# Kernel optimization log

Hardware: AMD Instinct MI355X
Metric: run time of the kernel (lower is better)

Reference implementation:

```python
import jax, jax.numpy as jnp
import numpy as np

N, IN_DIM, H, K = 4096, 64, 64, 3
DT = 0.05


def graph_filter(z, S_powers, W):
    # z: [N, d_in], S_powers: [K, N, N], W: [K, d_in, d_out]
    zk = jnp.einsum('knm,md->knd', S_powers, z)   # K-hop diffused features
    return jnp.einsum('knd,kde->ne', zk, W)       # sum over taps k


def setup_inputs() -> dict:
    key = jax.random.key(0)
    ks = jax.random.split(key, 8)
    w_scale = 0.1
    return {
        'x': jax.random.normal(ks[0], (N, H), jnp.float32),
        'u': jax.random.normal(ks[1], (N, IN_DIM), jnp.float32),
        'S_powers': jax.random.normal(ks[2], (K, N, N), jnp.float32) / np.float32(np.sqrt(N)),
        'WA_hat': jax.random.normal(ks[3], (K, H, H), jnp.float32) * w_scale,
        'WB_hat': jax.random.normal(ks[4], (K, IN_DIM, H), jnp.float32) * w_scale,
        'WA_state': jax.random.normal(ks[5], (K, H, H), jnp.float32) * w_scale,
        'WB_state': jax.random.normal(ks[6], (K, IN_DIM, H), jnp.float32) * w_scale,
        'bx': jnp.zeros((1, H), jnp.float32),
        'bu': jnp.zeros((1, H), jnp.float32),
        'b': jnp.ones((1, H), jnp.float32) * 0.1,
        'n_steps': 4,
    }


def reference(x, u, S_powers, WA_hat, WB_hat, WA_state, WB_state, bx, bu, b, n_steps):
    # Input-driven terms are constant across solver steps; hoist them.
    fu = jax.nn.relu(graph_filter(u, S_powers, WB_hat) + bu)   # [N, H]
    sigma_c = jnp.tanh(graph_filter(u, S_powers, WB_state))    # [N, H]

    def step(xc, _):
        f = jax.nn.relu(graph_filter(xc, S_powers, WA_hat) + bx) + fu
        dx = -(b + f) * xc - graph_filter(xc, S_powers, WA_state) + f * sigma_c
        xn = jnp.clip(xc + DT * dx, -1.0, 1.0)
        return xn, None

    xf, _ = jax.lax.scan(step, x, None, length=n_steps)
    return xf
```

## Files before the change

kernel.cpp:

```cpp
#include <hip/hip_runtime.h>
#include <math.h>


typedef unsigned short u16;
typedef unsigned int u32;
typedef __attribute__((ext_vector_type(8))) short short8;
typedef __attribute__((ext_vector_type(4))) float f32x4;

#define NN 4096
#define HD 64
#define KB32 128
#define DT_C 0.05f

__device__ __forceinline__ u16 f2bf(float f) {
    u32 u = __float_as_uint(f);
    u += 0x7FFFu + ((u >> 16) & 1u);
    return (u16)(u >> 16);
}
__device__ __forceinline__ u32 pk2(float a, float b) {
    return (u32)f2bf(a) | ((u32)f2bf(b) << 16);
}

__global__ __launch_bounds__(256) void zprep_kernel(
    const float* __restrict__ u, const float* __restrict__ x,
    const float* __restrict__ WAh, const float* __restrict__ WAs,
    const float* __restrict__ WBh, const float* __restrict__ WBs,
    u16* __restrict__ utT, u16* __restrict__ xtT, u16* __restrict__ WtT)
{
    const int b = blockIdx.x;
    const int t = threadIdx.x;
    if (b < 256) {
        const float* z = (b < 128) ? u : x;
        u16* ztT = (b < 128) ? utT : xtT;
        const int kb = b & 127, n0 = kb * 32;
        __shared__ __align__(16) u16 tile[64][40];
        const int nl = t >> 3, c0 = (t & 7) * 8;
        const float* src = z + (size_t)(n0 + nl) * HD + c0;
        float4 f0 = ((const float4*)src)[0];
        float4 f1 = ((const float4*)src)[1];
        tile[c0 + 0][nl] = f2bf(f0.x); tile[c0 + 1][nl] = f2bf(f0.y);
        tile[c0 + 2][nl] = f2bf(f0.z); tile[c0 + 3][nl] = f2bf(f0.w);
        tile[c0 + 4][nl] = f2bf(f1.x); tile[c0 + 5][nl] = f2bf(f1.y);
        tile[c0 + 6][nl] = f2bf(f1.z); tile[c0 + 7][nl] = f2bf(f1.w);
        __syncthreads();
        const int e = t >> 2, kw0 = (t & 3) * 8;
        short8 v = *(const short8*)&tile[e][kw0];
        *(short8*)(ztT + ((size_t)kb * 64 + e) * 32 + kw0) = v;
    } else {
        for (int f = t; f < 4 * 6 * 64 * 32; f += 256) {
            int mat = f / 12288, r = f % 12288;
            int s = r / 2048, r2 = r % 2048;
            int e = r2 >> 5, kw = r2 & 31;
            int kp = s * 32 + kw, tap = kp >> 6, d = kp & 63;
            const float* Wm = (mat == 0) ? WAh : (mat == 1) ? WAs : (mat == 2) ? WBh : WBs;
            WtT[f] = f2bf(Wm[((size_t)tap * HD + d) * HD + e]);
        }
    }
}

__global__ __launch_bounds__(256) void diffuseA_kernel(
    const float* __restrict__ S, const u16* __restrict__ utT,
    const u16* __restrict__ xtT, u16* __restrict__ SbT,
    float* __restrict__ Yp, int iters)
{
    const int t = threadIdx.x;
    const int tap = blockIdx.z;
    const int row0 = blockIdx.x * 128;
    const int kb0 = blockIdx.y * iters;
    const int w = t >> 6, lane = t & 63, l15 = lane & 15, quad = lane >> 4;

    const int r0 = row0 + w * 32 + l15;
    const float* Sb = S + ((size_t)tap * NN + r0) * NN + quad * 8;
    u16* Wb = SbT + (((size_t)tap * KB32) * NN + r0) * 32 + quad * 8;

    f32x4 z4 = {0.f, 0.f, 0.f, 0.f};
    f32x4 acc[2][2][4];
    #pragma unroll
    for (int s = 0; s < 2; ++s)
        #pragma unroll
        for (int i = 0; i < 2; ++i)
            #pragma unroll
            for (int j = 0; j < 4; ++j) acc[s][i][j] = z4;

    #pragma unroll 2
    for (int it = 0; it < iters; ++it) {
        const int kb = kb0 + it;
        const float* sp0 = Sb + (size_t)kb * 32;
        const float* sp1 = sp0 + (size_t)16 * NN;
        float4 f0 = ((const float4*)sp0)[0];
        float4 f1 = ((const float4*)sp0)[1];
        float4 g0 = ((const float4*)sp1)[0];
        float4 g1 = ((const float4*)sp1)[1];
        union U { uint4 u4; short8 s8; };
        U A0, A1;
        A0.u4.x = pk2(f0.x, f0.y); A0.u4.y = pk2(f0.z, f0.w);
        A0.u4.z = pk2(f1.x, f1.y); A0.u4.w = pk2(f1.z, f1.w);
        A1.u4.x = pk2(g0.x, g0.y); A1.u4.y = pk2(g0.z, g0.w);
        A1.u4.z = pk2(g1.x, g1.y); A1.u4.w = pk2(g1.z, g1.w);
        u16* wb = Wb + (size_t)kb * (NN * 32);
        *(uint4*)wb = A0.u4;
        *(uint4*)(wb + 16 * 32) = A1.u4;
        #pragma unroll
        for (int ct = 0; ct < 4; ++ct) {
            const size_t bo = ((size_t)kb * 64 + ct * 16 + l15) * 32 + quad * 8;
            short8 bu = *(const short8*)(utT + bo);
            short8 bx = *(const short8*)(xtT + bo);
            acc[0][0][ct] = __builtin_amdgcn_mfma_f32_16x16x32_bf16(A0.s8, bu, acc[0][0][ct], 0, 0, 0);
            acc[0][1][ct] = __builtin_amdgcn_mfma_f32_16x16x32_bf16(A1.s8, bu, acc[0][1][ct], 0, 0, 0);
            acc[1][0][ct] = __builtin_amdgcn_mfma_f32_16x16x32_bf16(A0.s8, bx, acc[1][0][ct], 0, 0, 0);
            acc[1][1][ct] = __builtin_amdgcn_mfma_f32_16x16x32_bf16(A1.s8, bx, acc[1][1][ct], 0, 0, 0);
        }
    }
    #pragma unroll
    for (int s = 0; s < 2; ++s) {
        float* yb = Yp + ((size_t)((blockIdx.y * 3 + tap) * 2 + s) * NN + row0) * HD;
        #pragma unroll
        for (int rt = 0; rt < 2; ++rt)
            #pragma unroll
            for (int ct = 0; ct < 4; ++ct)
                #pragma unroll
                for (int r = 0; r < 4; ++r)
                    yb[(size_t)(w * 32 + rt * 16 + quad * 4 + r) * HD + ct * 16 + l15] = acc[s][rt][ct][r];
    }
}

__global__ __launch_bounds__(256) void diffuseS_kernel(
    const u16* __restrict__ SbT, const u16* __restrict__ xtT,
    float* __restrict__ Yp, int iters)
{
    const int t = threadIdx.x;
    const int tap = blockIdx.z;
    const int row0 = blockIdx.x * 128;
    const int kb0 = blockIdx.y * iters;
    const int w = t >> 6, lane = t & 63, l15 = lane & 15, quad = lane >> 4;

    const u16* A0 = SbT + (((size_t)(tap * KB32) * NN + row0 + w * 32 + l15) * 32) + quad * 8;
    const size_t arowstride = (size_t)NN * 32;

    f32x4 z4 = {0.f, 0.f, 0.f, 0.f};
    f32x4 acc[2][4];
    #pragma unroll
    for (int i = 0; i < 2; ++i)
        #pragma unroll
        for (int j = 0; j < 4; ++j) acc[i][j] = z4;

    #pragma unroll 2
    for (int it = 0; it < iters; ++it) {
        const int kb = kb0 + it;
        const u16* ab = A0 + (size_t)kb * arowstride;
        short8 a0 = *(const short8*)(ab);
        short8 a1 = *(const short8*)(ab + 16 * 32);
        #pragma unroll
        for (int ct = 0; ct < 4; ++ct) {
            short8 bb = *(const short8*)(xtT + ((size_t)kb * 64 + ct * 16 + l15) * 32 + quad * 8);
            acc[0][ct] = __builtin_amdgcn_mfma_f32_16x16x32_bf16(a0, bb, acc[0][ct], 0, 0, 0);
            acc[1][ct] = __builtin_amdgcn_mfma_f32_16x16x32_bf16(a1, bb, acc[1][ct], 0, 0, 0);
        }
    }
    float* yb = Yp + ((size_t)(blockIdx.y * 3 + tap) * NN + row0) * HD;
    #pragma unroll
    for (int rt = 0; rt < 2; ++rt)
        #pragma unroll
        for (int ct = 0; ct < 4; ++ct)
            #pragma unroll
            for (int r = 0; r < 4; ++r)
                yb[(size_t)(w * 32 + rt * 16 + quad * 4 + r) * HD + ct * 16 + l15] = acc[rt][ct][r];
}

__global__ __launch_bounds__(256) void update_step_kernel(
    const float* __restrict__ Yp, int KS, const u16* __restrict__ WtT,
    const float* __restrict__ bx, const float* __restrict__ bvec,
    const float* __restrict__ fu, const float* __restrict__ sc,
    const float* __restrict__ xc, float* __restrict__ xn,
    u16* __restrict__ xtT, int do_pack)
{
    __shared__ __align__(16) u16 yt[6][16][56];
    __shared__ __align__(16) u16 pkt[64][24];
    const int t = threadIdx.x;
    const int n0 = blockIdx.x * 16;

    for (int f = t; f < 384; f += 256) {
        const int tap = f >> 7;
        const int r = f & 127;
        const int nl = r >> 3, d8 = r & 7, d0 = d8 * 8;
        const float* p = Yp + ((size_t)tap * NN + n0 + nl) * HD + d0;
        const size_t kstride = (size_t)3 * NN * HD;
        float4 s0 = {0.f, 0.f, 0.f, 0.f}, s1 = {0.f, 0.f, 0.f, 0.f};
        for (int y = 0; y < KS; ++y) {
            float4 v0 = ((const float4*)(p + (size_t)y * kstride))[0];
            float4 v1 = ((const float4*)(p + (size_t)y * kstride))[1];
            s0.x += v0.x; s0.y += v0.y; s0.z += v0.z; s0.w += v0.w;
            s1.x += v1.x; s1.y += v1.y; s1.z += v1.z; s1.w += v1.w;
        }
        uint4 o;
        o.x = pk2(s0.x, s0.y); o.y = pk2(s0.z, s0.w);
        o.z = pk2(s1.x, s1.y); o.w = pk2(s1.z, s1.w);
        const int s = tap * 2 + (d8 >> 2), kw0 = (d8 & 3) * 8;
        *(uint4*)&yt[s][nl][kw0] = o;
    }
    __syncthreads();

    const int wv = t >> 6, lane = t & 63, l15 = lane & 15, quad = lane >> 4;
    f32x4 z4 = {0.f, 0.f, 0.f, 0.f};
    f32x4 aF = z4, aG = z4;
    #pragma unroll
    for (int s = 0; s < 6; ++s) {
        short8 a = *(const short8*)&yt[s][l15][quad * 8];
        const size_t wo = ((size_t)s * 64 + wv * 16 + l15) * 32 + quad * 8;
        short8 bF = *(const short8*)(WtT + wo);
        short8 bG = *(const short8*)(WtT + wo + 12288);
        aF = __builtin_amdgcn_mfma_f32_16x16x32_bf16(a, bF, aF, 0, 0, 0);
        aG = __builtin_amdgcn_mfma_f32_16x16x32_bf16(a, bG, aG, 0, 0, 0);
    }
    const int e = wv * 16 + l15;
    const float bxv = bx[e], bbv = bvec[e];
    float xos[4];
    #pragma unroll
    for (int r = 0; r < 4; ++r) {
        const int n = n0 + quad * 4 + r;
        const size_t o = (size_t)n * HD + e;
        float ff = fmaxf(aF[r] + bxv, 0.f) + fu[o];
        float xv = xc[o];
        float dx = -(bbv + ff) * xv - aG[r] + ff * sc[o];
        float xo = fminf(fmaxf(xv + DT_C * dx, -1.f), 1.f);
        xn[o] = xo;
        xos[r] = xo;
    }
    if (do_pack) {
        uint2 pv;
        pv.x = pk2(xos[0], xos[1]);
        pv.y = pk2(xos[2], xos[3]);
        *(uint2*)&pkt[e][quad * 4] = pv;
        __syncthreads();
        if (t < 128) {
            const int ee = t >> 1, g = t & 1;
            short8 v = *(const short8*)&pkt[ee][g * 8];
            const int kb = n0 >> 5;
            const int kwb = (n0 & 31) + g * 8;
            *(short8*)(xtT + ((size_t)kb * 64 + ee) * 32 + kwb) = v;
        }
    }
}

__global__ __launch_bounds__(256) void update1_kernel(
    const float* __restrict__ Yp, int KS, const u16* __restrict__ WtT,
    const float* __restrict__ bx, const float* __restrict__ bu,
    const float* __restrict__ bvec, const float* __restrict__ x0,
    float* __restrict__ fu, float* __restrict__ sc, float* __restrict__ x1,
    u16* __restrict__ xtT)
{
    __shared__ __align__(16) u16 yt[2][6][16][56];
    __shared__ __align__(16) u16 pkt[64][24];
    const int t = threadIdx.x;
    const int n0 = blockIdx.x * 16;

    #pragma unroll
    for (int ff = 0; ff < 3; ++ff) {
        const int f = t + ff * 256;
        const int src = f / 384;
        const int r3 = f - src * 384;
        const int tap = r3 >> 7;
        const int r = r3 & 127;
        const int nl = r >> 3, d8 = r & 7, d0 = d8 * 8;
        const float* p = Yp + (((size_t)(tap * 2 + src)) * NN + n0 + nl) * HD + d0;
        const size_t kstride = (size_t)6 * NN * HD;
        float4 s0 = {0.f, 0.f, 0.f, 0.f}, s1 = {0.f, 0.f, 0.f, 0.f};
        for (int y = 0; y < KS; ++y) {
            float4 v0 = ((const float4*)(p + (size_t)y * kstride))[0];
            float4 v1 = ((const float4*)(p + (size_t)y * kstride))[1];
            s0.x += v0.x; s0.y += v0.y; s0.z += v0.z; s0.w += v0.w;
            s1.x += v1.x; s1.y += v1.y; s1.z += v1.z; s1.w += v1.w;
        }
        uint4 o;
        o.x = pk2(s0.x, s0.y); o.y = pk2(s0.z, s0.w);
        o.z = pk2(s1.x, s1.y); o.w = pk2(s1.z, s1.w);
        const int s = tap * 2 + (d8 >> 2), kw0 = (d8 & 3) * 8;
        *(uint4*)&yt[src][s][nl][kw0] = o;
    }
    __syncthreads();

    const int wv = t >> 6, lane = t & 63, l15 = lane & 15, quad = lane >> 4;
    f32x4 z4 = {0.f, 0.f, 0.f, 0.f};
    f32x4 aF = z4, aG = z4, aFu = z4, aSc = z4;
    #pragma unroll
    for (int s = 0; s < 6; ++s) {
        short8 au = *(const short8*)&yt[0][s][l15][quad * 8];
        short8 ax = *(const short8*)&yt[1][s][l15][quad * 8];
        const size_t wo = ((size_t)s * 64 + wv * 16 + l15) * 32 + quad * 8;
        short8 bF  = *(const short8*)(WtT + wo);
        short8 bG  = *(const short8*)(WtT + wo + 12288);
        short8 bFu = *(const short8*)(WtT + wo + 2 * 12288);
        short8 bSc = *(const short8*)(WtT + wo + 3 * 12288);
        aF  = __builtin_amdgcn_mfma_f32_16x16x32_bf16(ax, bF,  aF,  0, 0, 0);
        aG  = __builtin_amdgcn_mfma_f32_16x16x32_bf16(ax, bG,  aG,  0, 0, 0);
        aFu = __builtin_amdgcn_mfma_f32_16x16x32_bf16(au, bFu, aFu, 0, 0, 0);
        aSc = __builtin_amdgcn_mfma_f32_16x16x32_bf16(au, bSc, aSc, 0, 0, 0);
    }
    const int e = wv * 16 + l15;
    const float bxv = bx[e], buv = bu[e], bbv = bvec[e];
    float xos[4];
    #pragma unroll
    for (int r = 0; r < 4; ++r) {
        const int n = n0 + quad * 4 + r;
        const size_t o = (size_t)n * HD + e;
        float fuv = fmaxf(aFu[r] + buv, 0.f);
        float scv = tanhf(aSc[r]);
        float ff = fmaxf(aF[r] + bxv, 0.f) + fuv;
        float xv = x0[o];
        float dx = -(bbv + ff) * xv - aG[r] + ff * scv;
        float xo = fminf(fmaxf(xv + DT_C * dx, -1.f), 1.f);
        fu[o] = fuv; sc[o] = scv; x1[o] = xo;
        xos[r] = xo;
    }
    {
        uint2 pv;
        pv.x = pk2(xos[0], xos[1]);
        pv.y = pk2(xos[2], xos[3]);
        *(uint2*)&pkt[e][quad * 4] = pv;
        __syncthreads();
        if (t < 128) {
            const int ee = t >> 1, g = t & 1;
            short8 v = *(const short8*)&pkt[ee][g * 8];
            const int kb = n0 >> 5;
            const int kwb = (n0 & 31) + g * 8;
            *(short8*)(xtT + ((size_t)kb * 64 + ee) * 32 + kwb) = v;
        }
    }
}

extern "C" void kernel_launch(void* const* d_in, const int* in_sizes, int n_in,
                              void* d_out, int out_size, void* d_ws, size_t ws_size,
                              hipStream_t stream) {
    const float* x   = (const float*)d_in[0];
    const float* u   = (const float*)d_in[1];
    const float* S   = (const float*)d_in[2];
    const float* WAh = (const float*)d_in[3];
    const float* WBh = (const float*)d_in[4];
    const float* WAs = (const float*)d_in[5];
    const float* WBs = (const float*)d_in[6];
    const float* bx  = (const float*)d_in[7];
    const float* bu  = (const float*)d_in[8];
    const float* bvec= (const float*)d_in[9];
    float* out = (float*)d_out;

    const size_t sbf_bytes = (size_t)3 * NN * NN * 2;
    const size_t slice = (size_t)NN * HD * 4;
    const size_t rest = 2 * 524288 + 98304 + 4 * 1048576;
    int KS_A = 4, KS_S = 8, nslice = 24;
    if (ws_size < sbf_bytes + 24 * slice + rest) { KS_A = 2; KS_S = 4; nslice = 12; }
    if (ws_size < sbf_bytes + 12 * slice + rest) { KS_A = 1; KS_S = 2; nslice = 6; }

    char* p = (char*)d_ws;
    u16* SbT  = (u16*)p;         p += sbf_bytes;
    float* Yp = (float*)p;       p += (size_t)nslice * slice;
    u16* utT  = (u16*)p;         p += 524288;
    u16* xtT  = (u16*)p;         p += 524288;
    u16* WtT  = (u16*)p;         p += 98304;
    float* fu = (float*)p;       p += 1048576;
    float* sc = (float*)p;       p += 1048576;
    float* xA = (float*)p;       p += 1048576;
    float* xB = (float*)p;       p += 1048576;

    zprep_kernel<<<257, 256, 0, stream>>>(u, x, WAh, WAs, WBh, WBs, utT, xtT, WtT);

    diffuseA_kernel<<<dim3(32, KS_A, 3), 256, 0, stream>>>(S, utT, xtT, SbT, Yp, KB32 / KS_A);
    update1_kernel<<<256, 256, 0, stream>>>(Yp, KS_A, WtT, bx, bu, bvec, x, fu, sc, xA, xtT);

    diffuseS_kernel<<<dim3(32, KS_S, 3), 256, 0, stream>>>(SbT, xtT, Yp, KB32 / KS_S);
    update_step_kernel<<<256, 256, 0, stream>>>(Yp, KS_S, WtT, bx, bvec, fu, sc, xA, xB, xtT, 1);

    diffuseS_kernel<<<dim3(32, KS_S, 3), 256, 0, stream>>>(SbT, xtT, Yp, KB32 / KS_S);
    update_step_kernel<<<256, 256, 0, stream>>>(Yp, KS_S, WtT, bx, bvec, fu, sc, xB, xA, xtT, 1);

    diffuseS_kernel<<<dim3(32, KS_S, 3), 256, 0, stream>>>(SbT, xtT, Yp, KB32 / KS_S);
    update_step_kernel<<<256, 256, 0, stream>>>(Yp, KS_S, WtT, bx, bvec, fu, sc, xA, out, xtT, 0);
}
```

Baseline: 491.6 us.

## Stage diffusion B-operand tiles in LDS and raise split-K for first diffusion

Both diffusion kernels now copy 16 k-blocks of the transposed bf16 feature operands (u and x) into shared memory with a cooperative load. The MFMA loop then reads those operands from LDS instead of having each wave fetch them separately from global memory. The first diffusion kernel's split-K factor rises from 4 to 8, with a larger partial-sum buffer and a new fallback ladder keyed to workspace size. The cost is large dynamic LDS allocations (128 KB and 64 KB per block), which limit occupancy, and barriers with no double buffering between the stage and compute phases.

```diff
diff --git a/kernel.cpp b/kernel.cpp
--- a/kernel.cpp
+++ b/kernel.cpp
@@ -63,6 +63,7 @@
     const u16* __restrict__ xtT, u16* __restrict__ SbT,
     float* __restrict__ Yp, int iters)
 {
+    extern __shared__ __align__(16) u16 lds[];
     const int t = threadIdx.x;
     const int tap = blockIdx.z;
     const int row0 = blockIdx.x * 128;
@@ -82,33 +83,48 @@
             #pragma unroll
             for (int j = 0; j < 4; ++j) acc[s][i][j] = z4;
 
-    #pragma unroll 2
-    for (int it = 0; it < iters; ++it) {
-        const int kb = kb0 + it;
-        const float* sp0 = Sb + (size_t)kb * 32;
-        const float* sp1 = sp0 + (size_t)16 * NN;
-        float4 f0 = ((const float4*)sp0)[0];
-        float4 f1 = ((const float4*)sp0)[1];
-        float4 g0 = ((const float4*)sp1)[0];
-        float4 g1 = ((const float4*)sp1)[1];
-        union U { uint4 u4; short8 s8; };
-        U A0, A1;
-        A0.u4.x = pk2(f0.x, f0.y); A0.u4.y = pk2(f0.z, f0.w);
-        A0.u4.z = pk2(f1.x, f1.y); A0.u4.w = pk2(f1.z, f1.w);
-        A1.u4.x = pk2(g0.x, g0.y); A1.u4.y = pk2(g0.z, g0.w);
-        A1.u4.z = pk2(g1.x, g1.y); A1.u4.w = pk2(g1.z, g1.w);
-        u16* wb = Wb + (size_t)kb * (NN * 32);
-        *(uint4*)wb = A0.u4;
-        *(uint4*)(wb + 16 * 32) = A1.u4;
-        #pragma unroll
-        for (int ct = 0; ct < 4; ++ct) {
-            const size_t bo = ((size_t)kb * 64 + ct * 16 + l15) * 32 + quad * 8;
-            short8 bu = *(const short8*)(utT + bo);
-            short8 bx = *(const short8*)(xtT + bo);
-            acc[0][0][ct] = __builtin_amdgcn_mfma_f32_16x16x32_bf16(A0.s8, bu, acc[0][0][ct], 0, 0, 0);
-            acc[0][1][ct] = __builtin_amdgcn_mfma_f32_16x16x32_bf16(A1.s8, bu, acc[0][1][ct], 0, 0, 0);
-            acc[1][0][ct] = __builtin_amdgcn_mfma_f32_16x16x32_bf16(A0.s8, bx, acc[1][0][ct], 0, 0, 0);
-            acc[1][1][ct] = __builtin_amdgcn_mfma_f32_16x16x32_bf16(A1.s8, bx, acc[1][1][ct], 0, 0, 0);
+    for (int c0 = 0; c0 < iters; c0 += 16) {
+        __syncthreads();
+        for (int f = t; f < 8192; f += 256) {
+            const int src = f >> 12;
+            const int r = f & 4095;
+            const int kbr = r >> 8, ct = (r >> 6) & 3, ln = r & 63;
+            const int gkb = kb0 + c0 + kbr;
+            const u16* g = (src ? xtT : utT) +
+                ((size_t)(gkb * 64 + ct * 16 + (ln & 15))) * 32 + (ln >> 4) * 8;
+            *(short8*)&lds[(size_t)(((src * 16 + kbr) * 4 + ct) * 64 + ln) * 8] =
+                *(const short8*)g;
+        }
+        __syncthreads();
+
+        #pragma unroll 4
+        for (int kbr = 0; kbr < 16; ++kbr) {
+            const int kb = kb0 + c0 + kbr;
+            const float* sp0 = Sb + (size_t)kb * 32;
+            const float* sp1 = sp0 + (size_t)16 * NN;
+            float4 f0 = ((const float4*)sp0)[0];
+            float4 f1 = ((const float4*)sp0)[1];
+            float4 g0 = ((const float4*)sp1)[0];
+            float4 g1 = ((const float4*)sp1)[1];
+            union U { uint4 u4; short8 s8; };
+            U A0, A1;
+            A0.u4.x = pk2(f0.x, f0.y); A0.u4.y = pk2(f0.z, f0.w);
+            A0.u4.z = pk2(f1.x, f1.y); A0.u4.w = pk2(f1.z, f1.w);
+            A1.u4.x = pk2(g0.x, g0.y); A1.u4.y = pk2(g0.z, g0.w);
+            A1.u4.z = pk2(g1.x, g1.y); A1.u4.w = pk2(g1.z, g1.w);
+            u16* wb = Wb + (size_t)kb * (NN * 32);
+            *(uint4*)wb = A0.u4;
+            *(uint4*)(wb + 16 * 32) = A1.u4;
+            #pragma unroll
+            for (int ct = 0; ct < 4; ++ct) {
+                const int bo = ((kbr * 4 + ct) * 64 + lane) * 8;
+                short8 bu = *(const short8*)&lds[bo];
+                short8 bx = *(const short8*)&lds[32768 + bo];
+                acc[0][0][ct] = __builtin_amdgcn_mfma_f32_16x16x32_bf16(A0.s8, bu, acc[0][0][ct], 0, 0, 0);
+                acc[0][1][ct] = __builtin_amdgcn_mfma_f32_16x16x32_bf16(A1.s8, bu, acc[0][1][ct], 0, 0, 0);
+                acc[1][0][ct] = __builtin_amdgcn_mfma_f32_16x16x32_bf16(A0.s8, bx, acc[1][0][ct], 0, 0, 0);
+                acc[1][1][ct] = __builtin_amdgcn_mfma_f32_16x16x32_bf16(A1.s8, bx, acc[1][1][ct], 0, 0, 0);
+            }
         }
     }
     #pragma unroll
@@ -128,6 +144,7 @@
     const u16* __restrict__ SbT, const u16* __restrict__ xtT,
     float* __restrict__ Yp, int iters)
 {
+    extern __shared__ __align__(16) u16 lds[];
     const int t = threadIdx.x;
     const int tap = blockIdx.z;
     const int row0 = blockIdx.x * 128;
@@ -144,17 +161,29 @@
         #pragma unroll
         for (int j = 0; j < 4; ++j) acc[i][j] = z4;
 
-    #pragma unroll 2
-    for (int it = 0; it < iters; ++it) {
-        const int kb = kb0 + it;
-        const u16* ab = A0 + (size_t)kb * arowstride;
-        short8 a0 = *(const short8*)(ab);
-        short8 a1 = *(const short8*)(ab + 16 * 32);
-        #pragma unroll
-        for (int ct = 0; ct < 4; ++ct) {
-            short8 bb = *(const short8*)(xtT + ((size_t)kb * 64 + ct * 16 + l15) * 32 + quad * 8);
-            acc[0][ct] = __builtin_amdgcn_mfma_f32_16x16x32_bf16(a0, bb, acc[0][ct], 0, 0, 0);
-            acc[1][ct] = __builtin_amdgcn_mfma_f32_16x16x32_bf16(a1, bb, acc[1][ct], 0, 0, 0);
+    for (int c0 = 0; c0 < iters; c0 += 16) {
+        __syncthreads();
+        for (int f = t; f < 4096; f += 256) {
+            const int kbr = f >> 8, ct = (f >> 6) & 3, ln = f & 63;
+            const int gkb = kb0 + c0 + kbr;
+            const u16* g = xtT +
+                ((size_t)(gkb * 64 + ct * 16 + (ln & 15))) * 32 + (ln >> 4) * 8;
+            *(short8*)&lds[(size_t)((kbr * 4 + ct) * 64 + ln) * 8] = *(const short8*)g;
+        }
+        __syncthreads();
+
+        #pragma unroll 4
+        for (int kbr = 0; kbr < 16; ++kbr) {
+            const int kb = kb0 + c0 + kbr;
+            const u16* ab = A0 + (size_t)kb * arowstride;
+            short8 a0 = *(const short8*)(ab);
+            short8 a1 = *(const short8*)(ab + 16 * 32);
+            #pragma unroll
+            for (int ct = 0; ct < 4; ++ct) {
+                short8 bb = *(const short8*)&lds[((kbr * 4 + ct) * 64 + lane) * 8];
+                acc[0][ct] = __builtin_amdgcn_mfma_f32_16x16x32_bf16(a0, bb, acc[0][ct], 0, 0, 0);
+                acc[1][ct] = __builtin_amdgcn_mfma_f32_16x16x32_bf16(a1, bb, acc[1][ct], 0, 0, 0);
+            }
         }
     }
     float* yb = Yp + ((size_t)(blockIdx.y * 3 + tap) * NN + row0) * HD;
@@ -346,9 +375,11 @@
     const size_t sbf_bytes = (size_t)3 * NN * NN * 2;
     const size_t slice = (size_t)NN * HD * 4;
     const size_t rest = 2 * 524288 + 98304 + 4 * 1048576;
-    int KS_A = 4, KS_S = 8, nslice = 24;
-    if (ws_size < sbf_bytes + 24 * slice + rest) { KS_A = 2; KS_S = 4; nslice = 12; }
-    if (ws_size < sbf_bytes + 12 * slice + rest) { KS_A = 1; KS_S = 2; nslice = 6; }
+    int KS_A = 8, KS_S = 8;
+    if (ws_size < sbf_bytes + 48 * slice + rest) { KS_A = 4; KS_S = 8; }
+    if (ws_size < sbf_bytes + 24 * slice + rest) { KS_A = 2; KS_S = 4; }
+    if (ws_size < sbf_bytes + 12 * slice + rest) { KS_A = 1; KS_S = 2; }
+    const int nslice = (KS_A * 6 > KS_S * 3) ? KS_A * 6 : KS_S * 3;
 
     char* p = (char*)d_ws;
     u16* SbT  = (u16*)p;         p += sbf_bytes;
@@ -363,15 +394,15 @@
 
     zprep_kernel<<<257, 256, 0, stream>>>(u, x, WAh, WAs, WBh, WBs, utT, xtT, WtT);
 
-    diffuseA_kernel<<<dim3(32, KS_A, 3), 256, 0, stream>>>(S, utT, xtT, SbT, Yp, KB32 / KS_A);
+    diffuseA_kernel<<<dim3(32, KS_A, 3), 256, 131072, stream>>>(S, utT, xtT, SbT, Yp, KB32 / KS_A);
     update1_kernel<<<256, 256, 0, stream>>>(Yp, KS_A, WtT, bx, bu, bvec, x, fu, sc, xA, xtT);
 
-    diffuseS_kernel<<<dim3(32, KS_S, 3), 256, 0, stream>>>(SbT, xtT, Yp, KB32 / KS_S);
+    diffuseS_kernel<<<dim3(32, KS_S, 3), 256, 65536, stream>>>(SbT, xtT, Yp, KB32 / KS_S);
     update_step_kernel<<<256, 256, 0, stream>>>(Yp, KS_S, WtT, bx, bvec, fu, sc, xA, xB, xtT, 1);
 
-    diffuseS_kernel<<<dim3(32, KS_S, 3), 256, 0, stream>>>(SbT, xtT, Yp, KB32 / KS_S);
+    diffuseS_kernel<<<dim3(32, KS_S, 3), 256, 65536, stream>>>(SbT, xtT, Yp, KB32 / KS_S);
     update_step_kernel<<<256, 256, 0, stream>>>(Yp, KS_S, WtT, bx, bvec, fu, sc, xB, xA, xtT, 1);
 
-    diffuseS_kernel<<<dim3(32, KS_S, 3), 256, 0, stream>>>(SbT, xtT, Yp, KB32 / KS_S);
+    diffuseS_kernel<<<dim3(32, KS_S, 3), 256, 65536, stream>>>(SbT, xtT, Yp, KB32 / KS_S);
     update_step_kernel<<<256, 256, 0, stream>>>(Yp, KS_S, WtT, bx, bvec, fu, sc, xA, out, xtT, 0);
 }
```

After: 527.8 us. 1.07x slower.
